# Performance work log

Hardware: AMD Instinct MI355X
Metric: run time of the kernel (lower is better)

The kernel has to match this reference:

```python
import jax, jax.numpy as jnp
import numpy as np

N, E = 20000, 320000
IN, OUT, H1, H2 = 256, 32, 8, 1
NEG_SLOPE = 0.2


def _gatv2(x, src, dst, Wsrc, bsrc, Wdst, bdst, attn, Wres, bres, heads, dout):
    n = x.shape[0]
    fs = (x @ Wsrc + bsrc).reshape(n, heads, dout)   # (N,H,D)
    fd = (x @ Wdst + bdst).reshape(n, heads, dout)   # (N,H,D)
    # GATv2: leaky_relu BEFORE the attention dot product
    e = jax.nn.leaky_relu(fs[src] + fd[dst], NEG_SLOPE)      # (E,H,D)
    logits = jnp.einsum('ehd,hd->eh', e, attn)               # (E,H)
    # edge softmax over destination-node segments
    m = jax.ops.segment_max(logits, dst, num_segments=n)     # (N,H)
    ex = jnp.exp(logits - m[dst])
    s = jax.ops.segment_sum(ex, dst, num_segments=n)         # (N,H)
    alpha = ex / s[dst]                                      # (E,H)
    msg = alpha[:, :, None] * fs[src]                        # (E,H,D)
    out = jax.ops.segment_sum(msg, dst, num_segments=n)      # (N,H,D)
    res = (x @ Wres + bres).reshape(n, heads, dout)          # residual (dims differ -> Linear)
    return out + res


def setup_inputs() -> dict:
    key = jax.random.key(0)
    ks = jax.random.split(key, 16)
    sc = lambda fin: 1.0 / np.sqrt(fin)
    d = {}
    d['x'] = jax.random.normal(ks[0], (N, IN), jnp.float32)
    d['src'] = jax.random.randint(ks[1], (E,), 0, N, jnp.int32)
    d['dst'] = jax.random.randint(ks[2], (E,), 0, N, jnp.int32)
    # layer 1: IN -> OUT*H1
    d['Wsrc1'] = jax.random.normal(ks[3], (IN, OUT * H1), jnp.float32) * sc(IN)
    d['bsrc1'] = jnp.zeros((OUT * H1,), jnp.float32)
    d['Wdst1'] = jax.random.normal(ks[4], (IN, OUT * H1), jnp.float32) * sc(IN)
    d['bdst1'] = jnp.zeros((OUT * H1,), jnp.float32)
    d['attn1'] = jax.random.normal(ks[5], (H1, OUT), jnp.float32) * sc(OUT)
    d['Wres1'] = jax.random.normal(ks[6], (IN, OUT * H1), jnp.float32) * sc(IN)
    d['bres1'] = jnp.zeros((OUT * H1,), jnp.float32)
    # layer 2: OUT*H1 -> OUT, 1 head
    D2 = OUT * H1
    d['Wsrc2'] = jax.random.normal(ks[7], (D2, OUT * H2), jnp.float32) * sc(D2)
    d['bsrc2'] = jnp.zeros((OUT * H2,), jnp.float32)
    d['Wdst2'] = jax.random.normal(ks[8], (D2, OUT * H2), jnp.float32) * sc(D2)
    d['bdst2'] = jnp.zeros((OUT * H2,), jnp.float32)
    d['attn2'] = jax.random.normal(ks[9], (H2, OUT), jnp.float32) * sc(OUT)
    d['Wres2'] = jax.random.normal(ks[10], (D2, OUT * H2), jnp.float32) * sc(D2)
    d['bres2'] = jnp.zeros((OUT * H2,), jnp.float32)
    return d


def reference(x, src, dst,
              Wsrc1, bsrc1, Wdst1, bdst1, attn1, Wres1, bres1,
              Wsrc2, bsrc2, Wdst2, bdst2, attn2, Wres2, bres2):
    y = _gatv2(x, src, dst, Wsrc1, bsrc1, Wdst1, bdst1, attn1, Wres1, bres1, H1, OUT)
    y = jax.nn.relu(y)                       # (N, 8, OUT)
    y = y.reshape(x.shape[0], -1)            # (N, 8*OUT)
    y = _gatv2(y, src, dst, Wsrc2, bsrc2, Wdst2, bdst2, attn2, Wres2, bres2, H2, OUT)
    return y                                  # (N, 1, OUT)
```

## Files before the change

kernel.cpp:

```cpp
#include <hip/hip_runtime.h>
#include <hip/hip_bf16.h>

#define N_NODES 20000
#define N_PAD   20096
#define N_EDGES 320000
#define D_IN    256
#define NEG     0.2f
#define MAXDEG  64
#define NSB     64
#define EPSB    5000
#define NBIN    313

typedef __attribute__((ext_vector_type(8))) short short8;
typedef __attribute__((ext_vector_type(4))) float f32x4;
typedef __attribute__((ext_vector_type(4))) unsigned short u16x4;

__device__ __forceinline__ unsigned short f2b(float f) {
    unsigned int u = __float_as_uint(f);
    unsigned int r = (u + 0x7FFFu + ((u >> 16) & 1u)) >> 16;
    return (unsigned short)r;
}
__device__ __forceinline__ float b2f(unsigned short u) {
    union { unsigned int i; float f; } v;
    v.i = ((unsigned int)u) << 16;
    return v.f;
}

__device__ __forceinline__ void gload16(const void* g, void* l) {
    __builtin_amdgcn_global_load_lds((const __attribute__((address_space(1))) void*)g,
                                     (__attribute__((address_space(3))) void*)l, 16, 0, 0);
}

#define PB1 2512
#define PB2 3280
#define PB3 3376
#define PB4 3440
#define PREP_BLOCKS 3488
__global__ __launch_bounds__(256) void k_prep(
    const float* __restrict__ x, unsigned short* __restrict__ xb,
    const float* __restrict__ Ws1, const float* __restrict__ Wd1, const float* __restrict__ Wr1,
    unsigned short* __restrict__ wt,
    const float* __restrict__ Ws2, const float* __restrict__ Wd2, const float* __restrict__ Wr2,
    unsigned short* __restrict__ wt2,
    const int* __restrict__ dst, int* __restrict__ blockhist,
    unsigned short* __restrict__ yb)
{
    int bid = blockIdx.x, tid = threadIdx.x;
    if (bid < PB1) {
        int i = bid * 256 + tid;
        int row = i >> 5, c8 = (i & 31) * 8;
        short8 v = {0, 0, 0, 0, 0, 0, 0, 0};
        if (row < N_NODES) {
            float4 a = *reinterpret_cast<const float4*>(x + (size_t)row * 256 + c8);
            float4 b = *reinterpret_cast<const float4*>(x + (size_t)row * 256 + c8 + 4);
            v[0] = (short)f2b(a.x); v[1] = (short)f2b(a.y); v[2] = (short)f2b(a.z); v[3] = (short)f2b(a.w);
            v[4] = (short)f2b(b.x); v[5] = (short)f2b(b.y); v[6] = (short)f2b(b.z); v[7] = (short)f2b(b.w);
        }
        *reinterpret_cast<short8*>(xb + (size_t)row * 256 + c8) = v;
    } else if (bid < PB2) {
        int n = bid - PB1, k = tid;
        const float* W = (n < 256) ? Ws1 : ((n < 512) ? Wd1 : Wr1);
        int c = n & 255;
        wt[(size_t)n * 256 + k] = f2b(W[(size_t)k * 256 + c]);
    } else if (bid < PB3) {
        int n = bid - PB2, k = tid;
        const float* W = (n < 32) ? Ws2 : ((n < 64) ? Wd2 : Wr2);
        int c = n & 31;
        wt2[(size_t)n * 256 + (k ^ ((n & 7) << 3))] = f2b(W[(size_t)k * 32 + c]);
    } else if (bid < PB4) {
        __shared__ int hist[NBIN];
        int blk = bid - PB3;
        for (int b = tid; b < NBIN; b += 256) hist[b] = 0;
        __syncthreads();
        for (int it = 0; it < 20; ++it) {
            int li = it * 256 + tid;
            if (li < EPSB) atomicAdd(&hist[dst[blk * EPSB + li] >> 6], 1);
        }
        __syncthreads();
        for (int b = tid; b < NBIN; b += 256) blockhist[blk * NBIN + b] = hist[b];
    } else {
        int j = (bid - PB4) * 256 + tid;
        ((unsigned int*)(yb + (size_t)N_NODES * 256))[j] = 0u;
    }
}

__global__ __launch_bounds__(64) void k_pass2(const int* __restrict__ blockhist,
                                              int* __restrict__ start, int* __restrict__ bintotal)
{
    int bin = blockIdx.x, l = threadIdx.x;
    int v = blockhist[l * NBIN + bin];
    int xv = v;
    for (int off = 1; off < 64; off <<= 1) {
        int u = __shfl_up(xv, off);
        if (l >= off) xv += u;
    }
    start[l * NBIN + bin] = xv - v;
    if (l == 63) bintotal[bin] = xv;
}

__global__ __launch_bounds__(320) void k_pass3(
    const int* __restrict__ src, const int* __restrict__ dst,
    const int* __restrict__ start, const int* __restrict__ bintotal,
    unsigned long long* __restrict__ sorted, int* __restrict__ binbase_g)
{
    __shared__ int tmp[320];
    __shared__ int binbase[NBIN];
    __shared__ int rank[NBIN];
    int blk = blockIdx.x, tid = threadIdx.x;
    int bt = (tid < NBIN) ? bintotal[tid] : 0;
    tmp[tid] = bt;
    __syncthreads();
    for (int off = 1; off < 320; off <<= 1) {
        int v = (tid >= off) ? tmp[tid - off] : 0;
        __syncthreads();
        tmp[tid] += v;
        __syncthreads();
    }
    if (tid < NBIN) {
        int excl = tmp[tid] - bt;
        binbase[tid] = excl;
        rank[tid] = start[blk * NBIN + tid];
        if (blk == 0) binbase_g[tid] = excl;
    }
    __syncthreads();
    for (int it = 0; it < 16; ++it) {
        int li = it * 320 + tid;
        if (li < EPSB) {
            int e = blk * EPSB + li;
            int d = dst[e];
            int b = d >> 6;
            int r = atomicAdd(&rank[b], 1);
            sorted[binbase[b] + r] = ((unsigned long long)(unsigned)d << 32) | (unsigned)src[e];
        }
    }
}

__global__ __launch_bounds__(256) void k_pass4(
    const unsigned long long* __restrict__ sorted,
    const int* __restrict__ binbase_g, const int* __restrict__ bintotal,
    int* __restrict__ colp, int* __restrict__ cnt)
{
    __shared__ int ch[64];
    int nb = blockIdx.x, tid = threadIdx.x;
    if (tid < 64) ch[tid] = 0;
    __syncthreads();
    int base = binbase_g[nb], tot = bintotal[nb];
    for (int i = tid; i < tot; i += 256) {
        unsigned long long p = sorted[base + i];
        int d = (int)(p >> 32);
        int s = (int)(p & 0xffffffffULL);
        int r = atomicAdd(&ch[d & 63], 1);
        if (r < MAXDEG) colp[(size_t)d * MAXDEG + r] = s;
    }
    __syncthreads();
    int node = nb * 64 + tid;
    if (tid < 64 && node < N_NODES) cnt[node] = ch[tid];
}

#define GEMM1_BLOCKS 942
__global__ __launch_bounds__(256) void k_gemm_l1_mfma(
    const unsigned short* __restrict__ xb,
    const unsigned short* __restrict__ wt,
    const float* __restrict__ bs, const float* __restrict__ bd, const float* __restrict__ br,
    unsigned short* __restrict__ fs, unsigned short* __restrict__ fd, unsigned short* __restrict__ res)
{
    __shared__ __align__(16) unsigned short SH[2 * 128 * 64];
    int t = threadIdx.x;
    int bid = blockIdx.x;
    int lane = t & 63, w = t >> 6;
    const int q = 117, r = 6;
    int xcd = bid & 7, slot = bid >> 3;
    int wg = (xcd < r ? xcd * (q + 1) : r * (q + 1) + (xcd - r) * q) + slot;
    int mb = wg / 6, nb = wg % 6;
    int row0 = mb * 128;
    int which = nb >> 1;
    int col0 = (nb & 1) * 128;
    int ncol0 = nb * 128;
    unsigned short* out = (which == 0) ? fs : ((which == 1) ? fd : res);
    const float* bias   = (which == 0) ? bs : ((which == 1) ? bd : br);
    int wr = w >> 1, wc = w & 1;

    auto stage = [&](int buf, int k0) {
#pragma unroll
        for (int rnd = 0; rnd < 2; rnd++) {
            int c = rnd * 256 + t;
            int row = c >> 2, kc = (c & 3) * 8;
            char* base = (char*)SH + buf * 16384;
            gload16(xb + (size_t)(row0 + row) * 256 + k0 + kc, base + c * 16);
            gload16(wt + (size_t)(ncol0 + row) * 256 + k0 + kc, base + 8192 + c * 16);
        }
    };

    f32x4 acc[4][4] = {};

    stage(0, 0);
    __syncthreads();
    int cur = 0;
#pragma unroll
    for (int it = 0; it < 8; ++it) {
        if (it < 7) stage(cur ^ 1, (it + 1) * 32);
        const char* Ab = (const char*)SH + cur * 16384;
        const char* Bb = Ab + 8192;
        short8 a[4], b[4];
#pragma unroll
        for (int m = 0; m < 4; m++)
            a[m] = *reinterpret_cast<const short8*>(Ab + ((wr * 64 + m * 16 + (lane & 15)) * 64 + (lane >> 4) * 16));
#pragma unroll
        for (int n = 0; n < 4; n++)
            b[n] = *reinterpret_cast<const short8*>(Bb + ((wc * 64 + n * 16 + (lane & 15)) * 64 + (lane >> 4) * 16));
#pragma unroll
        for (int m = 0; m < 4; m++)
#pragma unroll
            for (int n = 0; n < 4; n++)
                acc[m][n] = __builtin_amdgcn_mfma_f32_16x16x32_bf16(a[m], b[n], acc[m][n], 0, 0, 0);
        __syncthreads();
        cur ^= 1;
    }

    int cgrp = lane >> 4, ccol = lane & 15;
    float bvals[4];
#pragma unroll
    for (int n = 0; n < 4; n++) bvals[n] = bias[col0 + wc * 64 + n * 16 + ccol];

#pragma unroll
    for (int p = 0; p < 2; p++) {
        if (p) __syncthreads();
        if (wr == p) {
#pragma unroll
            for (int m = 0; m < 4; m++)
#pragma unroll
                for (int n = 0; n < 4; n++)
#pragma unroll
                    for (int q2 = 0; q2 < 4; q2++) {
                        int lr = m * 16 + cgrp * 4 + q2;
                        int cb = (wc * 64 + n * 16 + ccol) * 2;
                        int addr = lr * 256 + (cb ^ (((lr >> 2) & 3) << 5));
                        *(unsigned short*)((char*)SH + addr) = f2b(acc[m][n][q2] + bvals[n]);
                    }
        }
        __syncthreads();
#pragma unroll
        for (int it = 0; it < 4; it++) {
            int lr = it * 16 + (t >> 4);
            int cb = (t & 15) * 16;
            short8 v = *(const short8*)((const char*)SH + (lr * 256 + (cb ^ (((lr >> 2) & 3) << 5))));
            int gr = row0 + p * 64 + lr;
            if (gr < N_NODES)
                *reinterpret_cast<short8*>(out + (size_t)gr * 256 + col0 + (t & 15) * 8) = v;
        }
    }
}

__global__ __launch_bounds__(64) void k_gather_l1(
    const int* __restrict__ cnt, const int* __restrict__ colp,
    const unsigned short* __restrict__ fs1, const unsigned short* __restrict__ fd1,
    const unsigned short* __restrict__ res1, const float* __restrict__ attn1,
    unsigned short* __restrict__ y)
{
    int n = blockIdx.x;
    int l = threadIdx.x;
    u16x4 fdv4 = *reinterpret_cast<const u16x4*>(fd1 + (size_t)n * 256 + l * 4);
    float fdv[4] = {b2f(fdv4[0]), b2f(fdv4[1]), b2f(fdv4[2]), b2f(fdv4[3])};
    float4 attv = *reinterpret_cast<const float4*>(attn1 + l * 4);
    float att[4] = {attv.x, attv.y, attv.z, attv.w};

    const int* colrow = colp + (size_t)n * MAXDEG;
    int deg = cnt[n];
    if (deg > MAXDEG) deg = MAXDEG;

    float m = -1e30f, s = 0.f;
    float acc[4] = {0.f, 0.f, 0.f, 0.f};
    int c0 = (0 < deg) ? colrow[0] : 0;
    int c1 = (1 < deg) ? colrow[1] : 0;
    u16x4 f0 = *reinterpret_cast<const u16x4*>(fs1 + (size_t)c0 * 256 + l * 4);
    u16x4 f1 = *reinterpret_cast<const u16x4*>(fs1 + (size_t)c1 * 256 + l * 4);
    for (int idx = 0; idx < deg; ++idx) {
        u16x4 fv4 = f0;
        f0 = f1;
        int c2 = (idx + 2 < deg) ? colrow[idx + 2] : 0;
        f1 = *reinterpret_cast<const u16x4*>(fs1 + (size_t)c2 * 256 + l * 4);
        float fv[4] = {b2f(fv4[0]), b2f(fv4[1]), b2f(fv4[2]), b2f(fv4[3])};
        float t0 = fv[0] + fdv[0]; t0 = t0 > 0.f ? t0 : NEG * t0;
        float t1 = fv[1] + fdv[1]; t1 = t1 > 0.f ? t1 : NEG * t1;
        float t2 = fv[2] + fdv[2]; t2 = t2 > 0.f ? t2 : NEG * t2;
        float t3 = fv[3] + fdv[3]; t3 = t3 > 0.f ? t3 : NEG * t3;
        float p = t0 * att[0] + t1 * att[1] + t2 * att[2] + t3 * att[3];
        p += __shfl_xor(p, 1);
        p += __shfl_xor(p, 2);
        p += __shfl_xor(p, 4);
        float mn = fmaxf(m, p);
        float e  = __expf(p - mn);
        float sc = __expf(m - mn);
        s = s * sc + e;
        acc[0] = acc[0] * sc + e * fv[0];
        acc[1] = acc[1] * sc + e * fv[1];
        acc[2] = acc[2] * sc + e * fv[2];
        acc[3] = acc[3] * sc + e * fv[3];
        m = mn;
    }
    u16x4 rv4 = *reinterpret_cast<const u16x4*>(res1 + (size_t)n * 256 + l * 4);
    float inv = (s > 0.f) ? 1.f / s : 0.f;
    u16x4 o;
    o[0] = f2b(fmaxf(acc[0] * inv + b2f(rv4[0]), 0.f));
    o[1] = f2b(fmaxf(acc[1] * inv + b2f(rv4[1]), 0.f));
    o[2] = f2b(fmaxf(acc[2] * inv + b2f(rv4[2]), 0.f));
    o[3] = f2b(fmaxf(acc[3] * inv + b2f(rv4[3]), 0.f));
    *reinterpret_cast<u16x4*>(y + (size_t)n * 256 + l * 4) = o;
}

__global__ __launch_bounds__(256) void k_gemm_l2_mfma(
    const unsigned short* __restrict__ yb,
    const unsigned short* __restrict__ wt2,
    const float* __restrict__ bs, const float* __restrict__ bd, const float* __restrict__ br,
    unsigned short* __restrict__ fs2, unsigned short* __restrict__ fd2, unsigned short* __restrict__ res2)
{
    __shared__ __align__(16) unsigned short Bs[96 * 256];
    __shared__ __align__(16) unsigned short As[2][64 * 32];
    int t = threadIdx.x;
    int lane = t & 63, w = t >> 6;
    int row0 = blockIdx.x * 64;

    auto stage_a = [&](int buf, int k0) {
        int c = t;
        int row = c >> 2, kc = (c & 3) * 8;
        gload16(yb + (size_t)(row0 + row) * 256 + k0 + kc, (char*)As[buf] + c * 16);
    };

#pragma unroll
    for (int i = 0; i < 12; i++) {
        int c = i * 256 + t;
        gload16(wt2 + (size_t)c * 8, (char*)Bs + (size_t)c * 16);
    }
    stage_a(0, 0);
    __syncthreads();

    f32x4 acc[6] = {};
    int arow0 = w * 16;
    int cur = 0;

#pragma unroll
    for (int it = 0; it < 8; ++it) {
        if (it < 7) stage_a(cur ^ 1, (it + 1) * 32);
        short8 a = *reinterpret_cast<const short8*>((const char*)As[cur] + ((arow0 + (lane & 15)) * 64 + (lane >> 4) * 16));
        short8 b[6];
#pragma unroll
        for (int n = 0; n < 6; n++) {
            int brow = n * 16 + (lane & 15);
            int kbyte = (it * 32 + (lane >> 4) * 8) * 2;
            b[n] = *reinterpret_cast<const short8*>((const char*)Bs + (brow * 512 + (kbyte ^ ((brow & 7) << 4))));
        }
#pragma unroll
        for (int n = 0; n < 6; n++)
            acc[n] = __builtin_amdgcn_mfma_f32_16x16x32_bf16(a, b[n], acc[n], 0, 0, 0);
        __syncthreads();
        cur ^= 1;
    }

    int cgrp = lane >> 4, ccol = lane & 15;
#pragma unroll
    for (int n = 0; n < 6; n++) {
        int which = n >> 1;
        int cc = (n & 1) * 16 + ccol;
        unsigned short* out = (which == 0) ? fs2 : ((which == 1) ? fd2 : res2);
        const float* bias   = (which == 0) ? bs  : ((which == 1) ? bd  : br);
        float bv = bias[cc];
        int rbase = row0 + arow0 + cgrp * 4;
#pragma unroll
        for (int q2 = 0; q2 < 4; q2++) {
            int rr = rbase + q2;
            if (rr < N_NODES) out[(size_t)rr * 32 + cc] = f2b(acc[n][q2] + bv);
        }
    }
}

__global__ __launch_bounds__(64) void k_gather_l2(
    const int* __restrict__ cnt, const int* __restrict__ colp,
    const unsigned short* __restrict__ fs2, const unsigned short* __restrict__ fd2,
    const unsigned short* __restrict__ res2, const float* __restrict__ attn2,
    float* __restrict__ out)
{
    int n = blockIdx.x;
    int l = threadIdx.x;
    int d = l & 31, h = l >> 5;
    float fdv = b2f(fd2[(size_t)n * 32 + d]);
    float att = attn2[d];
    const int* colrow = colp + (size_t)n * MAXDEG;
    int deg = cnt[n];
    if (deg > MAXDEG) deg = MAXDEG;

    float m = -1e30f, s = 0.f, acc = 0.f;
    int c0 = (h < deg) ? colrow[h] : 0;
    float fv_next = b2f(fs2[(size_t)c0 * 32 + d]);
    for (int i = h; i < deg; i += 2) {
        float fv = fv_next;
        int cn = (i + 2 < deg) ? colrow[i + 2] : 0;
        fv_next = b2f(fs2[(size_t)cn * 32 + d]);
        float t0 = fv + fdv; t0 = t0 > 0.f ? t0 : NEG * t0;
        float p = t0 * att;
        p += __shfl_xor(p, 1);
        p += __shfl_xor(p, 2);
        p += __shfl_xor(p, 4);
        p += __shfl_xor(p, 8);
        p += __shfl_xor(p, 16);
        float mn = fmaxf(m, p);
        float e  = __expf(p - mn);
        float sc = __expf(m - mn);
        s = s * sc + e;
        acc = acc * sc + e * fv;
        m = mn;
    }
    float mo = __shfl_xor(m, 32);
    float mstar = fmaxf(m, mo);
    float myc = __expf(m - mstar);
    float sp = s * myc, ap = acc * myc;
    float st = sp + __shfl_xor(sp, 32);
    float at = ap + __shfl_xor(ap, 32);
    if (l < 32) {
        float rv = b2f(res2[(size_t)n * 32 + d]);
        float inv = (st > 0.f) ? 1.f / st : 0.f;
        out[(size_t)n * 32 + d] = at * inv + rv;
    }
}

extern "C" void kernel_launch(void* const* d_in, const int* in_sizes, int n_in,
                              void* d_out, int out_size, void* d_ws, size_t ws_size,
                              hipStream_t stream)
{
    const float* x   = (const float*)d_in[0];
    const int*   src = (const int*)d_in[1];
    const int*   dst = (const int*)d_in[2];
    const float* Ws1 = (const float*)d_in[3];
    const float* bs1 = (const float*)d_in[4];
    const float* Wd1 = (const float*)d_in[5];
    const float* bd1 = (const float*)d_in[6];
    const float* at1 = (const float*)d_in[7];
    const float* Wr1 = (const float*)d_in[8];
    const float* br1 = (const float*)d_in[9];
    const float* Ws2 = (const float*)d_in[10];
    const float* bs2 = (const float*)d_in[11];
    const float* Wd2 = (const float*)d_in[12];
    const float* bd2 = (const float*)d_in[13];
    const float* at2 = (const float*)d_in[14];
    const float* Wr2 = (const float*)d_in[15];
    const float* br2 = (const float*)d_in[16];
    float* out = (float*)d_out;

    char* w = (char*)d_ws;
    size_t off = 0;
    auto alloc = [&](size_t bytes) { void* p = w + off; off += (bytes + 255) & ~(size_t)255; return p; };
    int*   cnt       = (int*)  alloc((size_t)N_NODES * 4);
    int*   colp      = (int*)  alloc((size_t)N_NODES * MAXDEG * 4);
    int*   blockhist = (int*)  alloc((size_t)NSB * NBIN * 4);
    int*   start     = (int*)  alloc((size_t)NSB * NBIN * 4);
    int*   bintotal  = (int*)  alloc((size_t)NBIN * 4);
    int*   binbase   = (int*)  alloc((size_t)NBIN * 4);
    unsigned long long* sorted = (unsigned long long*)alloc((size_t)N_EDGES * 8);
    unsigned short* fs1 = (unsigned short*)alloc((size_t)N_NODES * 256 * 2);
    unsigned short* fd1 = (unsigned short*)alloc((size_t)N_NODES * 256 * 2);
    unsigned short* res1= (unsigned short*)alloc((size_t)N_NODES * 256 * 2);
    unsigned short* fs2 = (unsigned short*)alloc((size_t)N_NODES * 32 * 2);
    unsigned short* fd2 = (unsigned short*)alloc((size_t)N_NODES * 32 * 2);
    unsigned short* res2= (unsigned short*)alloc((size_t)N_NODES * 32 * 2);
    unsigned short* xb  = (unsigned short*)alloc((size_t)N_PAD * 256 * 2);
    unsigned short* yb  = (unsigned short*)alloc((size_t)N_PAD * 256 * 2);
    unsigned short* wt  = (unsigned short*)alloc((size_t)768 * 256 * 2);
    unsigned short* wt2 = (unsigned short*)alloc((size_t)96 * 256 * 2);
    (void)ws_size; (void)in_sizes; (void)n_in; (void)out_size;

    k_prep<<<PREP_BLOCKS, 256, 0, stream>>>(x, xb, Ws1, Wd1, Wr1, wt, Ws2, Wd2, Wr2, wt2,
                                            dst, blockhist, yb);
    k_pass2<<<NBIN, 64, 0, stream>>>(blockhist, start, bintotal);
    k_pass3<<<NSB, 320, 0, stream>>>(src, dst, start, bintotal, sorted, binbase);
    k_pass4<<<NBIN, 256, 0, stream>>>(sorted, binbase, bintotal, colp, cnt);
    k_gemm_l1_mfma<<<GEMM1_BLOCKS, 256, 0, stream>>>(xb, wt, bs1, bd1, br1, fs1, fd1, res1);
    k_gather_l1<<<N_NODES, 64, 0, stream>>>(cnt, colp, fs1, fd1, res1, at1, yb);
    k_gemm_l2_mfma<<<N_PAD / 64, 256, 0, stream>>>(yb, wt2, bs2, bd2, br2, fs2, fd2, res2);
    k_gather_l2<<<N_NODES, 64, 0, stream>>>(cnt, colp, fs2, fd2, res2, at2, out);
}
```

Before: 111.0 us.

## Fold scan into pass3, merge CSR fill into GEMM launch, halve GEMM tile rows

Drops the separate pass2 scan kernel: each pass3 block now sums the per-block histograms itself to get its starting rank and the bin totals. The pass4 CSR fill is appended as extra blocks to the layer-1 GEMM launch, so both run in one dispatch and two launches disappear. The GEMM tile shrinks from 128 to 64 rows, doubling the block count and using less LDS per block. Each pass3 block now reads the whole histogram redundantly, and the smaller tiles reuse each weight load less.

```diff
diff --git a/kernel.cpp b/kernel.cpp
--- a/kernel.cpp
+++ b/kernel.cpp
@@ -84,31 +84,25 @@
     }
 }
 
-__global__ __launch_bounds__(64) void k_pass2(const int* __restrict__ blockhist,
-                                              int* __restrict__ start, int* __restrict__ bintotal)
-{
-    int bin = blockIdx.x, l = threadIdx.x;
-    int v = blockhist[l * NBIN + bin];
-    int xv = v;
-    for (int off = 1; off < 64; off <<= 1) {
-        int u = __shfl_up(xv, off);
-        if (l >= off) xv += u;
-    }
-    start[l * NBIN + bin] = xv - v;
-    if (l == 63) bintotal[bin] = xv;
-}
-
 __global__ __launch_bounds__(320) void k_pass3(
     const int* __restrict__ src, const int* __restrict__ dst,
-    const int* __restrict__ start, const int* __restrict__ bintotal,
-    unsigned long long* __restrict__ sorted, int* __restrict__ binbase_g)
+    const int* __restrict__ blockhist,
+    unsigned long long* __restrict__ sorted,
+    int* __restrict__ binbase_g, int* __restrict__ bintotal_g)
 {
     __shared__ int tmp[320];
     __shared__ int binbase[NBIN];
     __shared__ int rank[NBIN];
     int blk = blockIdx.x, tid = threadIdx.x;
-    int bt = (tid < NBIN) ? bintotal[tid] : 0;
-    tmp[tid] = bt;
+    int mystart = 0, total = 0;
+    if (tid < NBIN) {
+        for (int b = 0; b < NSB; ++b) {
+            int v = blockhist[b * NBIN + tid];
+            total += v;
+            if (b < blk) mystart += v;
+        }
+    }
+    tmp[tid] = (tid < NBIN) ? total : 0;
     __syncthreads();
     for (int off = 1; off < 320; off <<= 1) {
         int v = (tid >= off) ? tmp[tid - off] : 0;
@@ -117,10 +111,10 @@
         __syncthreads();
     }
     if (tid < NBIN) {
-        int excl = tmp[tid] - bt;
+        int excl = tmp[tid] - total;
         binbase[tid] = excl;
-        rank[tid] = start[blk * NBIN + tid];
-        if (blk == 0) binbase_g[tid] = excl;
+        rank[tid] = mystart;
+        if (blk == 0) { binbase_g[tid] = excl; bintotal_g[tid] = total; }
     }
     __syncthreads();
     for (int it = 0; it < 16; ++it) {
@@ -135,63 +129,66 @@
     }
 }
 
-__global__ __launch_bounds__(256) void k_pass4(
-    const unsigned long long* __restrict__ sorted,
-    const int* __restrict__ binbase_g, const int* __restrict__ bintotal,
-    int* __restrict__ colp, int* __restrict__ cnt)
-{
-    __shared__ int ch[64];
-    int nb = blockIdx.x, tid = threadIdx.x;
-    if (tid < 64) ch[tid] = 0;
-    __syncthreads();
-    int base = binbase_g[nb], tot = bintotal[nb];
-    for (int i = tid; i < tot; i += 256) {
-        unsigned long long p = sorted[base + i];
-        int d = (int)(p >> 32);
-        int s = (int)(p & 0xffffffffULL);
-        int r = atomicAdd(&ch[d & 63], 1);
-        if (r < MAXDEG) colp[(size_t)d * MAXDEG + r] = s;
-    }
-    __syncthreads();
-    int node = nb * 64 + tid;
-    if (tid < 64 && node < N_NODES) cnt[node] = ch[tid];
-}
-
-#define GEMM1_BLOCKS 942
+#define GEMM1_BLOCKS 1884
+#define PASS4_BLOCKS 313
 __global__ __launch_bounds__(256) void k_gemm_l1_mfma(
     const unsigned short* __restrict__ xb,
     const unsigned short* __restrict__ wt,
     const float* __restrict__ bs, const float* __restrict__ bd, const float* __restrict__ br,
-    unsigned short* __restrict__ fs, unsigned short* __restrict__ fd, unsigned short* __restrict__ res)
-{
-    __shared__ __align__(16) unsigned short SH[2 * 128 * 64];
+    unsigned short* __restrict__ fs, unsigned short* __restrict__ fd, unsigned short* __restrict__ res,
+    const unsigned long long* __restrict__ sorted,
+    const int* __restrict__ binbase_g, const int* __restrict__ bintotal_g,
+    int* __restrict__ colp, int* __restrict__ cnt)
+{
+    __shared__ __align__(16) unsigned short SH[12288];
     int t = threadIdx.x;
     int bid = blockIdx.x;
+
+    if (bid >= GEMM1_BLOCKS) {
+        int* ch = (int*)SH;
+        int nb2 = bid - GEMM1_BLOCKS;
+        if (t < 64) ch[t] = 0;
+        __syncthreads();
+        int base = binbase_g[nb2], tot = bintotal_g[nb2];
+        for (int i = t; i < tot; i += 256) {
+            unsigned long long p = sorted[base + i];
+            int d = (int)(p >> 32);
+            int s = (int)(p & 0xffffffffULL);
+            int r = atomicAdd(&ch[d & 63], 1);
+            if (r < MAXDEG) colp[(size_t)d * MAXDEG + r] = s;
+        }
+        __syncthreads();
+        int node = nb2 * 64 + t;
+        if (t < 64 && node < N_NODES) cnt[node] = ch[t];
+        return;
+    }
+
     int lane = t & 63, w = t >> 6;
-    const int q = 117, r = 6;
+    const int q = 235, r = 4;
     int xcd = bid & 7, slot = bid >> 3;
     int wg = (xcd < r ? xcd * (q + 1) : r * (q + 1) + (xcd - r) * q) + slot;
     int mb = wg / 6, nb = wg % 6;
-    int row0 = mb * 128;
+    int row0 = mb * 64;
     int which = nb >> 1;
     int col0 = (nb & 1) * 128;
     int ncol0 = nb * 128;
     unsigned short* out = (which == 0) ? fs : ((which == 1) ? fd : res);
     const float* bias   = (which == 0) ? bs : ((which == 1) ? bd : br);
-    int wr = w >> 1, wc = w & 1;
 
     auto stage = [&](int buf, int k0) {
-#pragma unroll
-        for (int rnd = 0; rnd < 2; rnd++) {
-            int c = rnd * 256 + t;
-            int row = c >> 2, kc = (c & 3) * 8;
-            char* base = (char*)SH + buf * 16384;
+        char* base = (char*)SH + buf * 12288;
+        {
+            int c = t, row = c >> 2, kc = (c & 3) * 8;
             gload16(xb + (size_t)(row0 + row) * 256 + k0 + kc, base + c * 16);
-            gload16(wt + (size_t)(ncol0 + row) * 256 + k0 + kc, base + 8192 + c * 16);
+        }
+#pragma unroll
+        for (int r2 = 0; r2 < 2; r2++) {
+            int c = r2 * 256 + t, row = c >> 2, kc = (c & 3) * 8;
+            gload16(wt + (size_t)(ncol0 + row) * 256 + k0 + kc, base + 4096 + c * 16);
         }
     };
 
-    f32x4 acc[4][4] = {};
+    f32x4 acc[4][2] = {};
 
     stage(0, 0);
     __syncthreads();
@@ -199,55 +196,49 @@
 #pragma unroll
     for (int it = 0; it < 8; ++it) {
         if (it < 7) stage(cur ^ 1, (it + 1) * 32);
-        const char* Ab = (const char*)SH + cur * 16384;
-        const char* Bb = Ab + 8192;
-        short8 a[4], b[4];
+        const char* Ab = (const char*)SH + cur * 12288;
+        const char* Bb = Ab + 4096;
+        short8 a[4], b[2];
 #pragma unroll
         for (int m = 0; m < 4; m++)
-            a[m] = *reinterpret_cast<const short8*>(Ab + ((wr * 64 + m * 16 + (lane & 15)) * 64 + (lane >> 4) * 16));
-#pragma unroll
-        for (int n = 0; n < 4; n++)
-            b[n] = *reinterpret_cast<const short8*>(Bb + ((wc * 64 + n * 16 + (lane & 15)) * 64 + (lane >> 4) * 16));
+            a[m] = *reinterpret_cast<const short8*>(Ab + ((m * 16 + (lane & 15)) * 64 + (lane >> 4) * 16));
+#pragma unroll
+        for (int n = 0; n < 2; n++)
+            b[n] = *reinterpret_cast<const short8*>(Bb + ((w * 32 + n * 16 + (lane & 15)) * 64 + (lane >> 4) * 16));
 #pragma unroll
         for (int m = 0; m < 4; m++)
 #pragma unroll
-            for (int n = 0; n < 4; n++)
+            for (int n = 0; n < 2; n++)
                 acc[m][n] = __builtin_amdgcn_mfma_f32_16x16x32_bf16(a[m], b[n], acc[m][n], 0, 0, 0);
         __syncthreads();
         cur ^= 1;
     }
 
     int cgrp = lane >> 4, ccol = lane & 15;
-    float bvals[4];
-#pragma unroll
-    for (int n = 0; n < 4; n++) bvals[n] = bias[col0 + wc * 64 + n * 16 + ccol];
-
-#pragma unroll
-    for (int p = 0; p < 2; p++) {
-        if (p) __syncthreads();
-        if (wr == p) {
-#pragma unroll
-            for (int m = 0; m < 4; m++)
-#pragma unroll
-                for (int n = 0; n < 4; n++)
-#pragma unroll
-                    for (int q2 = 0; q2 < 4; q2++) {
-                        int lr = m * 16 + cgrp * 4 + q2;
-                        int cb = (wc * 64 + n * 16 + ccol) * 2;
-                        int addr = lr * 256 + (cb ^ (((lr >> 2) & 3) << 5));
-                        *(unsigned short*)((char*)SH + addr) = f2b(acc[m][n][q2] + bvals[n]);
-                    }
-        }
-        __syncthreads();
-#pragma unroll
-        for (int it = 0; it < 4; it++) {
-            int lr = it * 16 + (t >> 4);
-            int cb = (t & 15) * 16;
-            short8 v = *(const short8*)((const char*)SH + (lr * 256 + (cb ^ (((lr >> 2) & 3) << 5))));
-            int gr = row0 + p * 64 + lr;
-            if (gr < N_NODES)
-                *reinterpret_cast<short8*>(out + (size_t)gr * 256 + col0 + (t & 15) * 8) = v;
-        }
+    float bvals[2];
+#pragma unroll
+    for (int n = 0; n < 2; n++) bvals[n] = bias[col0 + w * 32 + n * 16 + ccol];
+
+#pragma unroll
+    for (int m = 0; m < 4; m++)
+#pragma unroll
+        for (int n = 0; n < 2; n++)
+#pragma unroll
+            for (int q2 = 0; q2 < 4; q2++) {
+                int lr = m * 16 + cgrp * 4 + q2;
+                int cb = (w * 32 + n * 16 + ccol) * 2;
+                int addr = lr * 256 + (cb ^ (cgrp << 5));
+                *(unsigned short*)((char*)SH + addr) = f2b(acc[m][n][q2] + bvals[n]);
+            }
+    __syncthreads();
+#pragma unroll
+    for (int it = 0; it < 4; it++) {
+        int lr = it * 16 + (t >> 4);
+        int cb = (t & 15) * 16;
+        short8 v = *(const short8*)((const char*)SH + (lr * 256 + (cb ^ (((lr >> 2) & 3) << 5))));
+        int gr = row0 + lr;
+        if (gr < N_NODES)
+            *reinterpret_cast<short8*>(out + (size_t)gr * 256 + col0 + (t & 15) * 8) = v;
     }
 }
 
@@ -451,7 +442,6 @@
     int*   cnt       = (int*)  alloc((size_t)N_NODES * 4);
     int*   colp      = (int*)  alloc((size_t)N_NODES * MAXDEG * 4);
     int*   blockhist = (int*)  alloc((size_t)NSB * NBIN * 4);
-    int*   start     = (int*)  alloc((size_t)NSB * NBIN * 4);
     int*   bintotal  = (int*)  alloc((size_t)NBIN * 4);
     int*   binbase   = (int*)  alloc((size_t)NBIN * 4);
     unsigned long long* sorted = (unsigned long long*)alloc((size_t)N_EDGES * 8);
@@ -469,10 +459,9 @@
 
     k_prep<<<PREP_BLOCKS, 256, 0, stream>>>(x, xb, Ws1, Wd1, Wr1, wt, Ws2, Wd2, Wr2, wt2,
                                             dst, blockhist, yb);
-    k_pass2<<<NBIN, 64, 0, stream>>>(blockhist, start, bintotal);
-    k_pass3<<<NSB, 320, 0, stream>>>(src, dst, start, bintotal, sorted, binbase);
-    k_pass4<<<NBIN, 256, 0, stream>>>(sorted, binbase, bintotal, colp, cnt);
-    k_gemm_l1_mfma<<<GEMM1_BLOCKS, 256, 0, stream>>>(xb, wt, bs1, bd1, br1, fs1, fd1, res1);
+    k_pass3<<<NSB, 320, 0, stream>>>(src, dst, blockhist, sorted, binbase, bintotal);
+    k_gemm_l1_mfma<<<GEMM1_BLOCKS + PASS4_BLOCKS, 256, 0, stream>>>(
+        xb, wt, bs1, bd1, br1, fs1, fd1, res1, sorted, binbase, bintotal, colp, cnt);
     k_gather_l1<<<N_NODES, 64, 0, stream>>>(cnt, colp, fs1, fd1, res1, at1, yb);
     k_gemm_l2_mfma<<<N_PAD / 64, 256, 0, stream>>>(yb, wt2, bs2, bd2, br2, fs2, fd2, res2);
     k_gather_l2<<<N_NODES, 64, 0, stream>>>(cnt, colp, fs2, fd2, res2, at2, out);
```

Result: faster. 107.2 us (-3.4%).
